# Kernel tuning notes

Hardware: AMD Instinct MI355X
Metric: run time of the kernel (lower is better)

The kernel has to match this reference:

```python
import jax, jax.numpy as jnp
import numpy as np


def _lyndon_indices(c, d):
    """All Lyndon words of length <= d over alphabet {0..c-1} via Duval's algorithm,
    mapped to flat indices into the flattened signature (levels 1..d concatenated,
    first letter most significant within each level). Static numpy computation."""
    words = []
    w = [-1]
    while w:
        w[-1] += 1
        words.append(tuple(w))
        m = len(w)
        while len(w) < d:
            w.append(w[len(w) - m])
        while w and w[-1] == c - 1:
            w.pop()
    words.sort(key=lambda t: (len(t), t))  # group by word length, lexicographic within
    offsets = np.concatenate([[0], np.cumsum([c ** k for k in range(1, d + 1)])])
    idx = []
    for word in words:
        pos = 0
        for letter in word:
            pos = pos * c + letter
        idx.append(int(offsets[len(word) - 1]) + pos)
    return np.asarray(idx, dtype=np.int64)


def _split_levels(sig, c, d):
    levels, start = [], 0
    for k in range(1, d + 1):
        n = c ** k
        levels.append(sig[:, start:start + n])  # (B, c^k)
        start += n
    return levels


def _mul_by_S(P, S, d):
    """Graded product P (x) S in the truncated tensor algebra (zero scalar parts).
    P[i], S[i] are level-(i+1) components of shape (B, c^(i+1)) or None."""
    B = S[0].shape[0]
    out = [None] * d
    for m in range(d):  # output level m+1
        acc = None
        for i in range(m):  # P level i+1 combines with S level m-i
            if P[i] is None:
                continue
            t = jnp.einsum('bi,bj->bij', P[i], S[m - 1 - i]).reshape(B, -1)
            acc = t if acc is None else acc + t
        out[m] = acc
    return out


def _log_signature_flat(sig, c, d):
    """log(1 + S) truncated at depth d, flattened levels 1..d."""
    S = _split_levels(sig, c, d)
    L = list(S)  # n=1 term (coefficient +1)
    P = S
    for n in range(2, d + 1):
        P = _mul_by_S(P, S, d)  # P = S^{(x) n}, levels < n are None
        coef = ((-1.0) ** (n + 1)) / n
        for k in range(d):
            if P[k] is not None:
                L[k] = L[k] + coef * P[k]
    return jnp.concatenate(L, axis=1)


def setup_inputs() -> dict:
    key = jax.random.key(0)
    channels, depth, batch = 8, 6, 64
    width = sum(channels ** k for k in range(1, depth + 1))  # 299592
    signature = jax.random.normal(key, (batch, width), dtype=jnp.float32) * 0.1
    return {"signature": signature, "channels": channels, "depth": depth}


def reference(signature, channels, depth):
    idx = jnp.asarray(_lyndon_indices(channels, depth))
    log_sig = _log_signature_flat(signature, channels, depth)  # (B, width)
    return log_sig[:, idx]  # Lyndon-word coefficients ('words' mode)
```

## Files before the change

### kernel.cpp

```cpp
#include <hip/hip_runtime.h>

#define NWIDTH 299592
#define NOUT   51360

typedef unsigned long long ull;

__device__ const int g_B2[8] = {8, 15, 21, 26, 30, 33, 35, 36};
__device__ const int g_B3[8] = {36, 92, 134, 164, 184, 196, 202, 204};
__device__ const int g_B4[8] = {204, 624, 897, 1062, 1152, 1194, 1209, 1212};
__device__ const int g_B5[8] = {1212, 4404, 6210, 7140, 7560, 7716, 7758, 7764};
__device__ const int g_C6[7] = {0, 24052, 35861, 41016, 42926, 43480, 43587};

__device__ __forceinline__ bool is_lyndon6(unsigned p) {
  const unsigned mask = (1u << 18) - 1u;
#pragma unroll
  for (int k = 1; k < 6; ++k) {
    unsigned rot = ((p << (3 * k)) & mask) | (p >> (18 - 3 * k));
    if (p >= rot) return false;
  }
  return true;
}
__device__ __forceinline__ bool is_lyndon(unsigned p, int n) {
  const unsigned nb = 3u * (unsigned)n;
  const unsigned mask = (1u << nb) - 1u;
  for (int k = 1; k < n; ++k) {
    unsigned rot = ((p << (3 * k)) & mask) | (p >> (nb - 3 * k));
    if (p >= rot) return false;
  }
  return true;
}

__global__ __launch_bounds__(1024) void lyndon_prep(ull* __restrict__ mask64g,
                                                    int* __restrict__ grp_offg) {
  __shared__ unsigned LB[1024];
  __shared__ int ex[1024];
  __shared__ int wsum[16];
  const int tid = threadIdx.x, lane = tid & 63, wv = tid >> 6;
  const int j = blockIdx.x;
  const unsigned pb = ((unsigned)j << 15) | ((unsigned)tid << 5);
  unsigned lm = 0;
  int c = 0;
  for (int i = 0; i < 32; ++i) {
    if (is_lyndon6(pb | (unsigned)i)) { lm |= 1u << i; ++c; }
  }
  LB[tid] = lm;
  int pref = c;
  for (int d = 1; d < 64; d <<= 1) { int t = __shfl_up(pref, d); if (lane >= d) pref += t; }
  if (lane == 63) wsum[wv] = pref;
  __syncthreads();
  int base = 0;
  for (int i = 0; i < wv; ++i) base += wsum[i];
  ex[tid] = base + pref - c;
  __syncthreads();
  if (tid < 512) {
    ull m = (ull)LB[2 * tid] | ((ull)LB[2 * tid + 1] << 32);
    mask64g[j * 512 + tid] = m;
    grp_offg[j * 512 + tid] = g_C6[j] + ex[2 * tid];
  }
}

#define L_S3  0
#define L_S2  512
#define L_S1  576
#define L_PA  584
#define L_PB  1168
#define L_A2  1752
#define L_A3  1760
#define L_A4  1824
#define L_W4  2336
#define L_W5  2344
#define L_GO  2352
#define L_A5  2624
#define L_S4D 4672
#define L_MKD 8768
#define L_TOT 9280

__global__ __launch_bounds__(512)
void logsig_fused(const float* __restrict__ sig,
                  const ull* __restrict__ mask64g,
                  const int* __restrict__ grp_offg,
                  float* __restrict__ out) {
  __shared__ __align__(16) float sm[L_TOT];
  int* W4i = (int*)(sm + L_W4);
  int* W5i = (int*)(sm + L_W5);
  int* GOi = (int*)(sm + L_GO);
  ull* MKd = (ull*)(sm + L_MKD);

  const int tid = threadIdx.x, lane = tid & 63, wv = tid >> 6;
  const int bid = blockIdx.x;
  const int xcd = bid & 7;
  const int rr  = bid >> 3;
  const int b   = xcd * 8 + rr / 15;
  const int u   = rr % 15;
  const bool isalg = (u < 7);
  const int j1   = isalg ? u : ((u - 7) >> 1);
  const int half = isalg ? 0 : ((u - 7) & 1);

  const float* __restrict__ S   = sig + (size_t)b * NWIDTH;
  const float* __restrict__ S4g = S + 584;
  const float* __restrict__ S5g = S + 4680;
  const float* __restrict__ S6j = S + 37448 + (size_t)j1 * 32768;
  float* __restrict__ outb = out + (size_t)b * NOUT;

  const float p1 = S[j1];
  const float c2p1 = -0.5f * p1;
  const int q4 = tid << 2;

  ull sp_mk = 0; int sp_go = 0;
  if (isalg) {
    if (j1 >= 4) { sp_mk = mask64g[j1 * 512 + tid]; sp_go = grp_offg[j1 * 512 + tid]; }
  } else if (tid < 256) {
    MKd[tid] = mask64g[j1 * 512 + half * 256 + tid];
    GOi[tid] = grp_offg[j1 * 512 + half * 256 + tid];
  }
  sm[L_S3 + tid] = S[72 + tid];
  if (tid < 64) sm[L_S2 + tid] = S[8 + tid];
  if (tid < 8)  sm[L_S1 + tid] = S[tid];
  if (tid < 8)  sm[L_PA + tid]      = S[8 + j1 * 8 + tid];
  if (tid < 64) sm[L_PA + 8 + tid]  = S[72 + j1 * 64 + tid];
  sm[L_PA + 72 + tid] = S4g[j1 * 512 + tid];

  float p5[8];
  float a5[8] = {0.f, 0.f, 0.f, 0.f, 0.f, 0.f, 0.f, 0.f};
  float a4 = 0.f, a3 = 0.f, a2 = 0.f;
  if (isalg) {
    float4 va = *(const float4*)(S5g + j1 * 4096 + q4);
    float4 vb = *(const float4*)(S5g + j1 * 4096 + 2048 + q4);
    p5[0] = va.x; p5[1] = va.y; p5[2] = va.z; p5[3] = va.w;
    p5[4] = vb.x; p5[5] = vb.y; p5[6] = vb.z; p5[7] = vb.w;
  } else {
    float4 v = *(const float4*)(S5g + j1 * 4096 + half * 2048 + q4);
    p5[0] = v.x; p5[1] = v.y; p5[2] = v.z; p5[3] = v.w;
    *(float4*)(sm + L_S4D + tid * 8)     = *(const float4*)(S4g + tid * 8);
    *(float4*)(sm + L_S4D + tid * 8 + 4) = *(const float4*)(S4g + tid * 8 + 4);
  }

  ull m4 = 0;
  unsigned fm5a = 0, fm5b = 0;
  int exA = 0, exB = 0;
  if (isalg) {
    bool f4 = is_lyndon(((unsigned)j1 << 9) | (unsigned)tid, 4);
    m4 = __ballot(f4);
    if (lane == 0) W4i[wv] = __popcll(m4);
    int c5a = 0, c5b = 0;
#pragma unroll
    for (int e = 0; e < 4; ++e) {
      if (is_lyndon(((unsigned)j1 << 12) | (unsigned)(q4 + e), 5)) { fm5a |= 1u << e; ++c5a; }
      if (is_lyndon(((unsigned)j1 << 12) | (unsigned)(2048 + q4 + e), 5)) { fm5b |= 1u << e; ++c5b; }
    }
    int pk = c5a | (c5b << 16);
    int prefpk = pk;
    for (int d = 1; d < 64; d <<= 1) { int t = __shfl_up(prefpk, d); if (lane >= d) prefpk += t; }
    if (lane == 63) W5i[wv] = prefpk;
    exA = (prefpk & 0xffff) - c5a;
    exB = (prefpk >> 16) - c5b;
  }
  __syncthreads();

  const float s1t = sm[L_S1 + (tid & 7)];
  float s1q4[4];
#pragma unroll
  for (int e = 0; e < 4; ++e) s1q4[e] = sm[L_S1 + ((tid & 1) << 2) + e];

  const float coefs[7] = {0.f, 0.f, -0.5f, 1.f / 3.f, -0.25f, 0.2f, -1.f / 6.f};
#pragma unroll
  for (int n = 2; n <= 5; ++n) {
    const float coef = coefs[n];
    const int RP = (n & 1) ? L_PB : L_PA;
    const int WP = (n & 1) ? L_PA : L_PB;
    a4 += coef * sm[RP + 72 + tid];
    if (tid < 64) a3 += coef * sm[RP + 8 + tid];
    if (tid < 8)  a2 += coef * sm[RP + tid];
    float t4 = sm[RP + 8 + (tid >> 3)] * s1t
             + sm[RP + (tid >> 6)] * sm[L_S2 + (tid & 63)];
    if (n == 2) t4 += p1 * sm[L_S3 + tid];
    float t3 = 0.f, t2 = 0.f;
    if (tid < 64) {
      t3 = sm[RP + (tid >> 3)] * s1t;
      if (n == 2) t3 += p1 * sm[L_S2 + tid];
    }
    if (tid < 8 && n == 2) t2 = p1 * s1t;
    if (isalg) {
      const float rp4a = sm[RP + 72 + (tid >> 1)];
      const float rp4b = sm[RP + 72 + 256 + (tid >> 1)];
      const float rp3a = sm[RP + 8 + (tid >> 4)];
      const float rp3b = sm[RP + 8 + 32 + (tid >> 4)];
      const float rp2a = sm[RP + (tid >> 7)];
      const float rp2b = sm[RP + 4 + (tid >> 7)];
      const float4 s2v = *(const float4*)(sm + L_S2 + (q4 & 63));
      const float4 s3v = *(const float4*)(sm + L_S3 + (q4 & 511));
      const float s2q[4] = {s2v.x, s2v.y, s2v.z, s2v.w};
      const float s3q[4] = {s3v.x, s3v.y, s3v.z, s3v.w};
#pragma unroll
      for (int e = 0; e < 4; ++e) {
        a5[e]     += coef * p5[e];
        a5[4 + e] += coef * p5[4 + e];
        p5[e]     = rp4a * s1q4[e] + rp3a * s2q[e] + rp2a * s3q[e];
        p5[4 + e] = rp4b * s1q4[e] + rp3b * s2q[e] + rp2b * s3q[e];
      }
      if (n == 2) {
        const float4 s4va = *(const float4*)(S4g + q4);
        const float4 s4vb = *(const float4*)(S4g + 2048 + q4);
        const float s4qa[4] = {s4va.x, s4va.y, s4va.z, s4va.w};
        const float s4qb[4] = {s4vb.x, s4vb.y, s4vb.z, s4vb.w};
#pragma unroll
        for (int e = 0; e < 4; ++e) {
          p5[e] += p1 * s4qa[e];
          p5[4 + e] += p1 * s4qb[e];
        }
      }
    } else {
      const int q = half * 2048 + q4;
      const float rq4 = sm[RP + 72 + (q >> 3)];
      const float rq3 = sm[RP + 8 + (q >> 6)];
      const float rq2 = sm[RP + (q >> 9)];
      const float4 s2v = *(const float4*)(sm + L_S2 + (q & 63));
      const float4 s3v = *(const float4*)(sm + L_S3 + (q & 511));
      const float s2q[4] = {s2v.x, s2v.y, s2v.z, s2v.w};
      const float s3q[4] = {s3v.x, s3v.y, s3v.z, s3v.w};
#pragma unroll
      for (int e = 0; e < 4; ++e) {
        a5[e] += coef * p5[e];
        p5[e] = rq4 * s1q4[e] + rq3 * s2q[e] + rq2 * s3q[e];
      }
      if (n == 2) {
        const float4 s4v = *(const float4*)(sm + L_S4D + q);
        const float s4q[4] = {s4v.x, s4v.y, s4v.z, s4v.w};
#pragma unroll
        for (int e = 0; e < 4; ++e) p5[e] += p1 * s4q[e];
      }
    }
    sm[WP + 72 + tid] = t4;
    if (tid < 64) sm[WP + 8 + tid] = t3;
    if (tid < 8)  sm[WP + tid]     = t2;
    __syncthreads();
  }
#pragma unroll
  for (int e = 0; e < 8; ++e) a5[e] += coefs[6] * p5[e];

  sm[L_A4 + tid] = a4;
  if (tid < 64) sm[L_A3 + tid] = a3;
  if (tid < 8)  sm[L_A2 + tid] = a2;
  if (isalg) {
    *(float4*)(sm + L_A5 + q4)        = make_float4(a5[0], a5[1], a5[2], a5[3]);
    *(float4*)(sm + L_A5 + 2048 + q4) = make_float4(a5[4], a5[5], a5[6], a5[7]);
  } else {
    *(float4*)(sm + L_A5 + q4) = make_float4(a5[0], a5[1], a5[2], a5[3]);
  }
  __syncthreads();

  if (isalg) {
    float l2v = 0.f, l3v = 0.f;
    if (tid < 8)
      l2v = sm[L_S2 + j1 * 8 + tid] + c2p1 * s1t;
    if (tid < 64)
      l3v = sm[L_S3 + j1 * 64 + tid] + sm[L_A2 + (tid >> 3)] * s1t
          + c2p1 * sm[L_S2 + tid];
    const float l4v = S4g[j1 * 512 + tid] + sm[L_A3 + (tid >> 3)] * s1t
                    + sm[L_A2 + (tid >> 6)] * sm[L_S2 + (tid & 63)]
                    + c2p1 * sm[L_S3 + tid];
    float l5a[4], l5b[4];
    {
      const float4 via  = *(const float4*)(S5g + j1 * 4096 + q4);
      const float4 vib  = *(const float4*)(S5g + j1 * 4096 + 2048 + q4);
      const float4 s4va = *(const float4*)(S4g + q4);
      const float4 s4vb = *(const float4*)(S4g + 2048 + q4);
      const float4 s2v  = *(const float4*)(sm + L_S2 + (q4 & 63));
      const float4 s3v  = *(const float4*)(sm + L_S3 + (q4 & 511));
      const float l5ia[4] = {via.x, via.y, via.z, via.w};
      const float l5ib[4] = {vib.x, vib.y, vib.z, vib.w};
      const float s4qa[4] = {s4va.x, s4va.y, s4va.z, s4va.w};
      const float s4qb[4] = {s4vb.x, s4vb.y, s4vb.z, s4vb.w};
      const float s2q[4]  = {s2v.x, s2v.y, s2v.z, s2v.w};
      const float s3q[4]  = {s3v.x, s3v.y, s3v.z, s3v.w};
      const float a4a = sm[L_A4 + (tid >> 1)],  a4b = sm[L_A4 + 256 + (tid >> 1)];
      const float a3a = sm[L_A3 + (tid >> 4)],  a3b = sm[L_A3 + 32 + (tid >> 4)];
      const float a2a = sm[L_A2 + (tid >> 7)],  a2b = sm[L_A2 + 4 + (tid >> 7)];
#pragma unroll
      for (int e = 0; e < 4; ++e) {
        l5a[e] = l5ia[e] + a4a * s1q4[e] + a3a * s2q[e] + a2a * s3q[e] + c2p1 * s4qa[e];
        l5b[e] = l5ib[e] + a4b * s1q4[e] + a3b * s2q[e] + a2b * s3q[e] + c2p1 * s4qb[e];
      }
    }
    if (tid == 0) {
      outb[j1] = p1;
      if (j1 == 0) outb[7] = sm[L_S1 + 7];
    }
    if (tid < 8 && tid > j1) outb[g_B2[j1] + tid - j1 - 1] = l2v;
    if (tid < 64) {
      bool f3 = is_lyndon(((unsigned)j1 << 6) | (unsigned)tid, 3);
      ull m3 = __ballot(f3);
      if (f3) outb[g_B3[j1] + __popcll(m3 & ((1ull << lane) - 1ull))] = l3v;
    }
    {
      int base = 0;
      for (int i = 0; i < wv; ++i) base += W4i[i];
      if ((m4 >> lane) & 1ull)
        outb[g_B4[j1] + base + __popcll(m4 & ((1ull << lane) - 1ull))] = l4v;
    }
    {
      int baseA = 0, baseB = 0, totalA = 0;
#pragma unroll
      for (int i = 0; i < 8; ++i) {
        int w = W5i[i];
        totalA += w & 0xffff;
        if (i < wv) { baseA += w & 0xffff; baseB += w >> 16; }
      }
      int slotA = g_B5[j1] + baseA + exA;
      int slotB = g_B5[j1] + totalA + baseB + exB;
#pragma unroll
      for (int e = 0; e < 4; ++e)
        if ((fm5a >> e) & 1u) outb[slotA++] = l5a[e];
#pragma unroll
      for (int e = 0; e < 4; ++e)
        if ((fm5b >> e) & 1u) outb[slotB++] = l5b[e];
    }
    if (j1 >= 4) {
      ull m = sp_mk;
      int slot = 7764 + sp_go;
      const int g6 = tid << 6;
      while (m) {
        const int bit = __builtin_ctzll(m);
        const int pl = g6 + bit;
        float v = S6j[pl]
                + sm[L_A5 + (pl >> 3)] * sm[L_S1 + (pl & 7)]
                + sm[L_A4 + (pl >> 6)] * sm[L_S2 + (pl & 63)]
                + sm[L_A3 + (pl >> 9)] * sm[L_S3 + (pl & 511)]
                + sm[L_A2 + (pl >> 12)] * S4g[pl & 4095]
                + c2p1 * S5g[pl];
        outb[slot++] = v;
        m &= m - 1;
      }
    }
  } else {
    const int pbase = half * 16384;
#pragma unroll 4
    for (int it = 0; it < 8; ++it) {
      const int pl0 = it * 2048 + q4;
      const int pg  = pbase + pl0;
      const int gl  = pl0 >> 6;
      const ull m   = MKd[gl];
      const int gofs = GOi[gl];
      const float4 x6 = *(const float4*)(S6j + pg);
      const float4 x5 = *(const float4*)(S5g + pg);
      const float x6a[4] = {x6.x, x6.y, x6.z, x6.w};
      const float x5a[4] = {x5.x, x5.y, x5.z, x5.w};
      const float a5v = sm[L_A5 + (pl0 >> 3)];
      const float a4v = sm[L_A4 + (pg >> 6)];
      const float a3v = sm[L_A3 + (pg >> 9)];
      const float a2v = sm[L_A2 + (pg >> 12)];
      const int c63 = pl0 & 63;
      const float4 s2v = *(const float4*)(sm + L_S2 + c63);
      const float4 s3v = *(const float4*)(sm + L_S3 + (pl0 & 511));
      const float4 s4v = *(const float4*)(sm + L_S4D + (pl0 & 4095));
      const float s2a[4] = {s2v.x, s2v.y, s2v.z, s2v.w};
      const float s3a[4] = {s3v.x, s3v.y, s3v.z, s3v.w};
      const float s4a[4] = {s4v.x, s4v.y, s4v.z, s4v.w};
#pragma unroll
      for (int e = 0; e < 4; ++e) {
        float v = x6a[e]
                + a5v * s1q4[e]
                + a4v * s2a[e]
                + a3v * s3a[e]
                + a2v * s4a[e]
                + c2p1 * x5a[e];
        if ((m >> (c63 + e)) & 1ull)
          outb[7764 + gofs + __popcll(m & ((1ull << (c63 + e)) - 1ull))] = v;
      }
    }
  }
}


extern "C" void kernel_launch(void* const* d_in, const int* in_sizes, int n_in,
                              void* d_out, int out_size, void* d_ws, size_t ws_size,
                              hipStream_t stream) {
  const float* sig = (const float*)d_in[0];
  float* out = (float*)d_out;
  ull* mask64g = (ull*)d_ws;
  int* grp_offg = (int*)(mask64g + 3584);

  lyndon_prep<<<7, 1024, 0, stream>>>(mask64g, grp_offg);
  logsig_fused<<<960, 512, 0, stream>>>(sig, mask64g, grp_offg, out);
}
```

Before: 41.28 us.

## Compact level-6 Lyndon positions into a list and rebalance blocks over outputs

The prep kernel now writes a compacted list of 16-bit level-6 Lyndon positions instead of per-group bitmasks and offsets. The main kernel splits the level-6 work into ranges balanced by output count across 16 blocks per batch row rather than 15, and iterates only over Lyndon positions, each writing to a contiguous output slot. This is meant to remove wasted lanes on dense float4 loads for discarded words, the mask popcount logic, and the imbalance between level-6 slices. In exchange, every block now redoes the full level-5 recurrence, and the remaining level-6 reads are scattered gathers.

```diff
diff --git a/kernel.cpp b/kernel.cpp
--- a/kernel.cpp
+++ b/kernel.cpp
@@ -4,12 +4,16 @@
 #define NOUT   51360
 
 typedef unsigned long long ull;
+typedef unsigned short u16;
 
 __device__ const int g_B2[8] = {8, 15, 21, 26, 30, 33, 35, 36};
 __device__ const int g_B3[8] = {36, 92, 134, 164, 184, 196, 202, 204};
 __device__ const int g_B4[8] = {204, 624, 897, 1062, 1152, 1194, 1209, 1212};
 __device__ const int g_B5[8] = {1212, 4404, 6210, 7140, 7560, 7716, 7758, 7764};
-__device__ const int g_C6[7] = {0, 24052, 35861, 41016, 42926, 43480, 43587};
+__device__ const int g_C6[8] = {0, 24052, 35861, 41016, 42926, 43480, 43587, 43596};
+__device__ const int g_dj1[9] = {0, 0, 0, 0, 0, 1, 1, 2, 3};
+__device__ const int g_dr0[9] = {0, 4811, 9622, 14432, 19242, 24052, 29957, 35861, 41016};
+__device__ const int g_dr1[9] = {4811, 9622, 14432, 19242, 24052, 29957, 35861, 41016, 42926};
 
 __device__ __forceinline__ bool is_lyndon6(unsigned p) {
   const unsigned mask = (1u << 18) - 1u;
@@ -30,32 +34,28 @@
   return true;
 }
 
-__global__ __launch_bounds__(1024) void lyndon_prep(ull* __restrict__ mask64g,
-                                                    int* __restrict__ grp_offg) {
-  __shared__ unsigned LB[1024];
-  __shared__ int ex[1024];
+__global__ __launch_bounds__(1024) void lyndon_prep(u16* __restrict__ pos16) {
   __shared__ int wsum[16];
   const int tid = threadIdx.x, lane = tid & 63, wv = tid >> 6;
   const int j = blockIdx.x;
   const unsigned pb = ((unsigned)j << 15) | ((unsigned)tid << 5);
   unsigned lm = 0;
   int c = 0;
-  for (int i = 0; i < 32; ++i) {
+  for (int i = 0; i < 32; ++i)
     if (is_lyndon6(pb | (unsigned)i)) { lm |= 1u << i; ++c; }
-  }
-  LB[tid] = lm;
   int pref = c;
   for (int d = 1; d < 64; d <<= 1) { int t = __shfl_up(pref, d); if (lane >= d) pref += t; }
   if (lane == 63) wsum[wv] = pref;
   __syncthreads();
   int base = 0;
   for (int i = 0; i < wv; ++i) base += wsum[i];
-  ex[tid] = base + pref - c;
-  __syncthreads();
-  if (tid < 512) {
-    ull m = (ull)LB[2 * tid] | ((ull)LB[2 * tid + 1] << 32);
-    mask64g[j * 512 + tid] = m;
-    grp_offg[j * 512 + tid] = g_C6[j] + ex[2 * tid];
+  int ex = g_C6[j] + base + pref - c;
+  unsigned m = lm;
+  const int p0 = tid << 5;
+  while (m) {
+    const int bit = __builtin_ctz(m);
+    pos16[ex++] = (u16)(p0 + bit);
+    m &= m - 1;
   }
 }
 
@@ -69,32 +69,36 @@
 #define L_A4  1824
 #define L_W4  2336
 #define L_W5  2344
-#define L_GO  2352
-#define L_A5  2624
-#define L_S4D 4672
-#define L_MKD 8768
-#define L_TOT 9280
+#define L_A5  2352
+#define L_PL  6448
+#define L_TOT 9404
 
 __global__ __launch_bounds__(512)
 void logsig_fused(const float* __restrict__ sig,
-                  const ull* __restrict__ mask64g,
-                  const int* __restrict__ grp_offg,
+                  const u16* __restrict__ pos16,
                   float* __restrict__ out) {
   __shared__ __align__(16) float sm[L_TOT];
   int* W4i = (int*)(sm + L_W4);
   int* W5i = (int*)(sm + L_W5);
-  int* GOi = (int*)(sm + L_GO);
-  ull* MKd = (ull*)(sm + L_MKD);
+  u16* PL  = (u16*)(sm + L_PL);
 
   const int tid = threadIdx.x, lane = tid & 63, wv = tid >> 6;
   const int bid = blockIdx.x;
   const int xcd = bid & 7;
   const int rr  = bid >> 3;
-  const int b   = xcd * 8 + rr / 15;
-  const int u   = rr % 15;
+  const int b   = xcd * 8 + (rr >> 4);
+  const int u   = rr & 15;
   const bool isalg = (u < 7);
-  const int j1   = isalg ? u : ((u - 7) >> 1);
-  const int half = isalg ? 0 : ((u - 7) & 1);
+  const int j1 = isalg ? u : g_dj1[u - 7];
+  int r0, r1;
+  if (isalg) {
+    r0 = (j1 >= 4) ? g_C6[j1] : 0;
+    r1 = (j1 >= 4) ? g_C6[j1 + 1] : 0;
+  } else {
+    r0 = g_dr0[u - 7];
+    r1 = g_dr1[u - 7];
+  }
+  const int cnt = r1 - r0;
 
   const float* __restrict__ S   = sig + (size_t)b * NWIDTH;
   const float* __restrict__ S4g = S + 584;
@@ -106,34 +110,22 @@
   const float c2p1 = -0.5f * p1;
   const int q4 = tid << 2;
 
-  ull sp_mk = 0; int sp_go = 0;
-  if (isalg) {
-    if (j1 >= 4) { sp_mk = mask64g[j1 * 512 + tid]; sp_go = grp_offg[j1 * 512 + tid]; }
-  } else if (tid < 256) {
-    MKd[tid] = mask64g[j1 * 512 + half * 256 + tid];
-    GOi[tid] = grp_offg[j1 * 512 + half * 256 + tid];
-  }
   sm[L_S3 + tid] = S[72 + tid];
   if (tid < 64) sm[L_S2 + tid] = S[8 + tid];
   if (tid < 8)  sm[L_S1 + tid] = S[tid];
   if (tid < 8)  sm[L_PA + tid]      = S[8 + j1 * 8 + tid];
   if (tid < 64) sm[L_PA + 8 + tid]  = S[72 + j1 * 64 + tid];
   sm[L_PA + 72 + tid] = S4g[j1 * 512 + tid];
-
+  for (int i = tid; i < cnt; i += 512) PL[i] = pos16[r0 + i];
   float p5[8];
-  float a5[8] = {0.f, 0.f, 0.f, 0.f, 0.f, 0.f, 0.f, 0.f};
-  float a4 = 0.f, a3 = 0.f, a2 = 0.f;
-  if (isalg) {
+  {
     float4 va = *(const float4*)(S5g + j1 * 4096 + q4);
     float4 vb = *(const float4*)(S5g + j1 * 4096 + 2048 + q4);
     p5[0] = va.x; p5[1] = va.y; p5[2] = va.z; p5[3] = va.w;
     p5[4] = vb.x; p5[5] = vb.y; p5[6] = vb.z; p5[7] = vb.w;
-  } else {
-    float4 v = *(const float4*)(S5g + j1 * 4096 + half * 2048 + q4);
-    p5[0] = v.x; p5[1] = v.y; p5[2] = v.z; p5[3] = v.w;
-    *(float4*)(sm + L_S4D + tid * 8)     = *(const float4*)(S4g + tid * 8);
-    *(float4*)(sm + L_S4D + tid * 8 + 4) = *(const float4*)(S4g + tid * 8 + 4);
-  }
+  }
+  float a5[8] = {0.f, 0.f, 0.f, 0.f, 0.f, 0.f, 0.f, 0.f};
+  float a4 = 0.f, a3 = 0.f, a2 = 0.f;
 
   ull m4 = 0;
   unsigned fm5a = 0, fm5b = 0;
@@ -148,8 +140,7 @@
       if (is_lyndon(((unsigned)j1 << 12) | (unsigned)(q4 + e), 5)) { fm5a |= 1u << e; ++c5a; }
       if (is_lyndon(((unsigned)j1 << 12) | (unsigned)(2048 + q4 + e), 5)) { fm5b |= 1u << e; ++c5b; }
     }
-    int pk = c5a | (c5b << 16);
-    int prefpk = pk;
+    int prefpk = c5a | (c5b << 16);
     for (int d = 1; d < 64; d <<= 1) { int t = __shfl_up(prefpk, d); if (lane >= d) prefpk += t; }
     if (lane == 63) W5i[wv] = prefpk;
     exA = (prefpk & 0xffff) - c5a;
@@ -180,7 +171,7 @@
       if (n == 2) t3 += p1 * sm[L_S2 + tid];
     }
     if (tid < 8 && n == 2) t2 = p1 * s1t;
-    if (isalg) {
+    {
       const float rp4a = sm[RP + 72 + (tid >> 1)];
       const float rp4b = sm[RP + 72 + 256 + (tid >> 1)];
       const float rp3a = sm[RP + 8 + (tid >> 4)];
@@ -209,26 +200,6 @@
           p5[4 + e] += p1 * s4qb[e];
         }
       }
-    } else {
-      const int q = half * 2048 + q4;
-      const float rq4 = sm[RP + 72 + (q >> 3)];
-      const float rq3 = sm[RP + 8 + (q >> 6)];
-      const float rq2 = sm[RP + (q >> 9)];
-      const float4 s2v = *(const float4*)(sm + L_S2 + (q & 63));
-      const float4 s3v = *(const float4*)(sm + L_S3 + (q & 511));
-      const float s2q[4] = {s2v.x, s2v.y, s2v.z, s2v.w};
-      const float s3q[4] = {s3v.x, s3v.y, s3v.z, s3v.w};
-#pragma unroll
-      for (int e = 0; e < 4; ++e) {
-        a5[e] += coef * p5[e];
-        p5[e] = rq4 * s1q4[e] + rq3 * s2q[e] + rq2 * s3q[e];
-      }
-      if (n == 2) {
-        const float4 s4v = *(const float4*)(sm + L_S4D + q);
-        const float s4q[4] = {s4v.x, s4v.y, s4v.z, s4v.w};
-#pragma unroll
-        for (int e = 0; e < 4; ++e) p5[e] += p1 * s4q[e];
-      }
     }
     sm[WP + 72 + tid] = t4;
     if (tid < 64) sm[WP + 8 + tid] = t3;
@@ -241,12 +212,8 @@
   sm[L_A4 + tid] = a4;
   if (tid < 64) sm[L_A3 + tid] = a3;
   if (tid < 8)  sm[L_A2 + tid] = a2;
-  if (isalg) {
-    *(float4*)(sm + L_A5 + q4)        = make_float4(a5[0], a5[1], a5[2], a5[3]);
-    *(float4*)(sm + L_A5 + 2048 + q4) = make_float4(a5[4], a5[5], a5[6], a5[7]);
-  } else {
-    *(float4*)(sm + L_A5 + q4) = make_float4(a5[0], a5[1], a5[2], a5[3]);
-  }
+  *(float4*)(sm + L_A5 + q4)        = make_float4(a5[0], a5[1], a5[2], a5[3]);
+  *(float4*)(sm + L_A5 + 2048 + q4) = make_float4(a5[4], a5[5], a5[6], a5[7]);
   __syncthreads();
 
   if (isalg) {
@@ -315,59 +282,17 @@
       for (int e = 0; e < 4; ++e)
         if ((fm5b >> e) & 1u) outb[slotB++] = l5b[e];
     }
-    if (j1 >= 4) {
-      ull m = sp_mk;
-      int slot = 7764 + sp_go;
-      const int g6 = tid << 6;
-      while (m) {
-        const int bit = __builtin_ctzll(m);
-        const int pl = g6 + bit;
-        float v = S6j[pl]
-                + sm[L_A5 + (pl >> 3)] * sm[L_S1 + (pl & 7)]
-                + sm[L_A4 + (pl >> 6)] * sm[L_S2 + (pl & 63)]
-                + sm[L_A3 + (pl >> 9)] * sm[L_S3 + (pl & 511)]
-                + sm[L_A2 + (pl >> 12)] * S4g[pl & 4095]
-                + c2p1 * S5g[pl];
-        outb[slot++] = v;
-        m &= m - 1;
-      }
-    }
-  } else {
-    const int pbase = half * 16384;
-#pragma unroll 4
-    for (int it = 0; it < 8; ++it) {
-      const int pl0 = it * 2048 + q4;
-      const int pg  = pbase + pl0;
-      const int gl  = pl0 >> 6;
-      const ull m   = MKd[gl];
-      const int gofs = GOi[gl];
-      const float4 x6 = *(const float4*)(S6j + pg);
-      const float4 x5 = *(const float4*)(S5g + pg);
-      const float x6a[4] = {x6.x, x6.y, x6.z, x6.w};
-      const float x5a[4] = {x5.x, x5.y, x5.z, x5.w};
-      const float a5v = sm[L_A5 + (pl0 >> 3)];
-      const float a4v = sm[L_A4 + (pg >> 6)];
-      const float a3v = sm[L_A3 + (pg >> 9)];
-      const float a2v = sm[L_A2 + (pg >> 12)];
-      const int c63 = pl0 & 63;
-      const float4 s2v = *(const float4*)(sm + L_S2 + c63);
-      const float4 s3v = *(const float4*)(sm + L_S3 + (pl0 & 511));
-      const float4 s4v = *(const float4*)(sm + L_S4D + (pl0 & 4095));
-      const float s2a[4] = {s2v.x, s2v.y, s2v.z, s2v.w};
-      const float s3a[4] = {s3v.x, s3v.y, s3v.z, s3v.w};
-      const float s4a[4] = {s4v.x, s4v.y, s4v.z, s4v.w};
-#pragma unroll
-      for (int e = 0; e < 4; ++e) {
-        float v = x6a[e]
-                + a5v * s1q4[e]
-                + a4v * s2a[e]
-                + a3v * s3a[e]
-                + a2v * s4a[e]
-                + c2p1 * x5a[e];
-        if ((m >> (c63 + e)) & 1ull)
-          outb[7764 + gofs + __popcll(m & ((1ull << (c63 + e)) - 1ull))] = v;
-      }
-    }
+  }
+
+  for (int i = tid; i < cnt; i += 512) {
+    const int pl = PL[i];
+    float v = S6j[pl]
+            + sm[L_A5 + (pl >> 3)] * sm[L_S1 + (pl & 7)]
+            + sm[L_A4 + (pl >> 6)] * sm[L_S2 + (pl & 63)]
+            + sm[L_A3 + (pl >> 9)] * sm[L_S3 + (pl & 511)]
+            + sm[L_A2 + (pl >> 12)] * S4g[pl & 4095]
+            + c2p1 * S5g[pl];
+    outb[7764 + r0 + i] = v;
   }
 }
 
@@ -377,9 +302,8 @@
                               hipStream_t stream) {
   const float* sig = (const float*)d_in[0];
   float* out = (float*)d_out;
-  ull* mask64g = (ull*)d_ws;
-  int* grp_offg = (int*)(mask64g + 3584);
-
-  lyndon_prep<<<7, 1024, 0, stream>>>(mask64g, grp_offg);
-  logsig_fused<<<960, 512, 0, stream>>>(sig, mask64g, grp_offg, out);
-}
+  u16* pos16 = (u16*)d_ws;
+
+  lyndon_prep<<<7, 1024, 0, stream>>>(pos16);
+  logsig_fused<<<1024, 512, 0, stream>>>(sig, pos16, out);
+}
```

Result: no change. 41.56 us (+0.7%).
